# Kernel optimization log

Measured on AMD Instinct MI355X. Metric: run time of the kernel, lower is better.

## Reference

```python
import jax, jax.numpy as jnp
import numpy as np

LN_EPS = 1e-5

def setup_inputs() -> dict:
    key = jax.random.key(0)
    k1, k2, k3 = jax.random.split(key, 3)
    B, Lq, Lk, D = 16, 2048, 2048, 128
    return {
        "query": jax.random.normal(k1, (B, Lq, D), dtype=jnp.float32),
        "key": jax.random.normal(k2, (B, Lk, D), dtype=jnp.float32),
        "value": jax.random.normal(k3, (B, Lk, D), dtype=jnp.float32),
        "attn_mask": jnp.zeros((Lq, Lk), dtype=jnp.float32),
        "gamma": jnp.ones((D,), dtype=jnp.float32),
        "beta": jnp.zeros((D,), dtype=jnp.float32),
    }

def reference(query, key, value, attn_mask, gamma, beta):
    # NOTE: original code does NOT scale by 1/sqrt(d) despite the class name.
    scores = jnp.einsum("bqd,bkd->bqk", query, key)          # [B,Lq,Lk]
    scores = scores + attn_mask[None, :, :]
    probs = jax.nn.softmax(scores, axis=-1)
    out = jnp.einsum("bqk,bkd->bqd", probs, value)            # [B,Lq,D]
    # dropout is identity (eval / rate 0)
    mu = jnp.mean(out, axis=-1, keepdims=True)
    var = jnp.var(out, axis=-1, keepdims=True)
    normed = (out - mu) * jax.lax.rsqrt(var + LN_EPS)
    return normed * gamma + beta
```

## Files before the change

kernel.cpp:

```cpp
#include <hip/hip_runtime.h>
#include <hip/hip_bf16.h>
#include <math.h>

#define LQ_  2048
#define LK_  2048
#define D_   128
#define B_   16
#define LN_EPS 1e-5f
#define TK_  32
#define NTILE (LK_ / TK_)

#define KH_TILE_US 4096
#define VT_TILE_U  2048
#define KH_BYTES   ((size_t)B_ * NTILE * KH_TILE_US * 2)
#define VT_OFF     (2 * KH_BYTES)

typedef __attribute__((ext_vector_type(8))) short short8;
typedef __attribute__((ext_vector_type(4))) float f32x4;

union FragU { uint4 u4; short8 s8; unsigned int u[4]; };

__device__ __forceinline__ unsigned int pk_bf16(float a, float b) {
  __hip_bfloat162 h = __float22bfloat162_rn(make_float2(a, b));
  unsigned int u;
  __builtin_memcpy(&u, &h, 4);
  return u;
}
__device__ __forceinline__ float bf_lo(unsigned int u){ unsigned int v = u << 16; float f; __builtin_memcpy(&f, &v, 4); return f; }
__device__ __forceinline__ float bf_hi(unsigned int u){ unsigned int v = u & 0xffff0000u; float f; __builtin_memcpy(&f, &v, 4); return f; }
__device__ __forceinline__ unsigned short bf16_bits(float x) {
  return (unsigned short)(pk_bf16(x, 0.f) & 0xffffu);
}

__device__ __forceinline__ int idxK(int row, int d) {
  return row * 128 + ((((d >> 3) ^ row) & 15) << 3) + (d & 7);
}
__device__ __forceinline__ int idxVt(int d, int kp) {
  return d * 16 + ((((kp >> 2) + (d >> 1)) & 3) << 2) + (kp & 3);
}
__device__ __forceinline__ int idxPs(int row, int col) {
  return row * 32 + ((((col >> 3) ^ (row >> 2)) & 3) << 3) + (col & 7);
}

__device__ __forceinline__ void barrier_lds() {
  asm volatile("s_waitcnt lgkmcnt(0)\n\ts_barrier" ::: "memory");
}
__device__ __forceinline__ void barrier_stage() {
  asm volatile("s_waitcnt vmcnt(8) lgkmcnt(0)\n\ts_barrier" ::: "memory");
}

__device__ __forceinline__ void gld_lds16(const void* g, void* l) {
  __builtin_amdgcn_global_load_lds((const __attribute__((address_space(1))) void*)g,
                                   (__attribute__((address_space(3))) void*)l, 16, 0, 0);
}

__global__ __launch_bounds__(256) void conv_kv(
    const float* __restrict__ kg, const float* __restrict__ vg,
    unsigned short* __restrict__ khg, unsigned short* __restrict__ klg,
    unsigned int* __restrict__ vtg)
{
  __shared__ float Vlt[128 * 33];
  const int tid = threadIdx.x;
  const int blk = blockIdx.x;
  const int b = blk >> 6;
  const int t = blk & 63;

  const float* ks = kg + ((size_t)b * LK_ + t * 32) * D_;
  const float* vs = vg + ((size_t)b * LK_ + t * 32) * D_;
  unsigned short* kh = khg + (size_t)blk * KH_TILE_US;
  unsigned short* kl = klg + (size_t)blk * KH_TILE_US;
  unsigned int*   vt = vtg + (size_t)blk * VT_TILE_U;

#pragma unroll
  for (int it = 0; it < 2; it++) {
    const int item = tid + it * 256;
    const int row = item >> 4;
    const int c8  = item & 15;
    const float* p = ks + row * D_ + c8 * 8;
    float4 x = *(const float4*)(p);
    float4 y = *(const float4*)(p + 4);
    FragU H, L;
    H.u[0] = pk_bf16(x.x, x.y); H.u[1] = pk_bf16(x.z, x.w);
    H.u[2] = pk_bf16(y.x, y.y); H.u[3] = pk_bf16(y.z, y.w);
    L.u[0] = pk_bf16(x.x - bf_lo(H.u[0]), x.y - bf_hi(H.u[0]));
    L.u[1] = pk_bf16(x.z - bf_lo(H.u[1]), x.w - bf_hi(H.u[1]));
    L.u[2] = pk_bf16(y.x - bf_lo(H.u[2]), y.y - bf_hi(H.u[2]));
    L.u[3] = pk_bf16(y.z - bf_lo(H.u[3]), y.w - bf_hi(H.u[3]));
    const int ik = idxK(row, c8 * 8);
    *(uint4*)&kh[ik] = H.u4;
    *(uint4*)&kl[ik] = L.u4;
  }

#pragma unroll
  for (int i = 0; i < 4; i++) {
    const int item = tid + i * 256;
    const int r = item >> 5, c4 = item & 31;
    float4 x = *(const float4*)&vs[r * D_ + c4 * 4];
    Vlt[(c4 * 4 + 0) * 33 + r] = x.x;
    Vlt[(c4 * 4 + 1) * 33 + r] = x.y;
    Vlt[(c4 * 4 + 2) * 33 + r] = x.z;
    Vlt[(c4 * 4 + 3) * 33 + r] = x.w;
  }
  __syncthreads();

#pragma unroll
  for (int i = 0; i < 8; i++) {
    const int o = tid + i * 256;
    const int d = o >> 4, s = o & 15;
    const int gq = s >> 2, c = s & 3;
    const int kp = (((gq - (d >> 1)) & 3) << 2) | c;
    vt[o] = pk_bf16(Vlt[d * 33 + 2 * kp], Vlt[d * 33 + 2 * kp + 1]);
  }
}

__device__ __forceinline__ void stage_tile(int w, int lane,
    const unsigned short* khT, const unsigned short* klT, const unsigned int* vtT,
    int tile, unsigned short* khs, unsigned short* kls, unsigned int* vts)
{
  const char* gkh = (const char*)(khT + (size_t)tile * KH_TILE_US);
  const char* gkl = (const char*)(klT + (size_t)tile * KH_TILE_US);
  const char* gvt = (const char*)(vtT + (size_t)tile * VT_TILE_U);
#pragma unroll
  for (int c = 0; c < 2; c++) {
    const int off = (w + 4 * c) << 10;
    gld_lds16(gkh + off + lane * 16, (char*)khs + off);
    gld_lds16(gkl + off + lane * 16, (char*)kls + off);
    gld_lds16(gvt + off + lane * 16, (char*)vts + off);
  }
}

__global__ __launch_bounds__(256, 2) void attn_ln_mfma(
    const float* __restrict__ qg, const float* __restrict__ maskg,
    const float* __restrict__ gammag, const float* __restrict__ betag,
    const unsigned short* __restrict__ khg, const unsigned short* __restrict__ klg,
    const unsigned int* __restrict__ vtg,
    float* __restrict__ outg)
{
  __shared__ unsigned short KhS[2][32 * 128];
  __shared__ unsigned short KlS[2][32 * 128];
  __shared__ unsigned int   VtW[2][128 * 16];
  __shared__ unsigned short PsS[64 * 32];

  float* lExch = (float*)&PsS[0];
  float* sExch = ((float*)&PsS[0]) + 128;

  const int tid  = threadIdx.x;
  const int w    = tid >> 6;
  const int lane = tid & 63;
  const int quad = lane >> 4;
  const int lr   = lane & 15;
  const int rowgrp = w & 1;
  const int khalf  = w >> 1;

  const int id   = blockIdx.x;
  const int xcd  = id & 7;
  const int slot = id >> 3;
  const int b    = xcd * 2 + (slot >> 5);
  const int q0   = (slot & 31) * 64;

  const unsigned short* khT = khg + (size_t)b * NTILE * KH_TILE_US;
  const unsigned short* klT = klg + (size_t)b * NTILE * KH_TILE_US;
  const unsigned int*   vtT = vtg + (size_t)b * NTILE * VT_TILE_U;

  const float* mbase = maskg + (size_t)(q0 + rowgrp * 32 + quad * 4) * LK_ + khalf * 16 + lr;

  stage_tile(w, lane, khT, klT, vtT, 0, &KhS[0][0], &KlS[0][0], &VtW[0][0]);
  float mA[2][4], mB[2][4];
#pragma unroll
  for (int rt = 0; rt < 2; rt++)
#pragma unroll
    for (int reg = 0; reg < 4; reg++)
      mA[rt][reg] = mbase[(size_t)(rt * 16 + reg) * LK_];

  short8 qh[2][4], ql[2][4];
#pragma unroll
  for (int rt = 0; rt < 2; rt++) {
    const float* qrow = qg + ((size_t)b * LQ_ + q0 + rowgrp * 32 + rt * 16 + lr) * D_ + quad * 8;
#pragma unroll
    for (int c = 0; c < 4; c++) {
      float4 x = *(const float4*)(qrow + c * 32);
      float4 y = *(const float4*)(qrow + c * 32 + 4);
      FragU H, L;
      H.u[0] = pk_bf16(x.x, x.y); H.u[1] = pk_bf16(x.z, x.w);
      H.u[2] = pk_bf16(y.x, y.y); H.u[3] = pk_bf16(y.z, y.w);
      L.u[0] = pk_bf16(x.x - bf_lo(H.u[0]), x.y - bf_hi(H.u[0]));
      L.u[1] = pk_bf16(x.z - bf_lo(H.u[1]), x.w - bf_hi(H.u[1]));
      L.u[2] = pk_bf16(y.x - bf_lo(H.u[2]), y.y - bf_hi(H.u[2]));
      L.u[3] = pk_bf16(y.z - bf_lo(H.u[3]), y.w - bf_hi(H.u[3]));
      qh[rt][c] = H.s8; ql[rt][c] = L.s8;
    }
  }

  float l_part[2][4];
  f32x4 o[2][4];
  const f32x4 zf = {0.f, 0.f, 0.f, 0.f};
#pragma unroll
  for (int rt = 0; rt < 2; rt++) {
#pragma unroll
    for (int r = 0; r < 4; r++) l_part[rt][r] = 0.f;
#pragma unroll
    for (int n = 0; n < 4; n++) o[rt][n] = zf;
  }

  auto body = [&](int kt, int cur, float (&mu)[2][4], float (&mp)[2][4])
      __attribute__((always_inline)) -> void {
    const unsigned short* khc = &KhS[cur][0];
    const unsigned short* klc = &KlS[cur][0];
    const unsigned int*   vtc = &VtW[cur][0];

    barrier_stage();

    if (kt + 1 < NTILE) {
      stage_tile(w, lane, khT, klT, vtT, kt + 1,
                 &KhS[cur ^ 1][0], &KlS[cur ^ 1][0], &VtW[cur ^ 1][0]);
#pragma unroll
      for (int rt = 0; rt < 2; rt++)
#pragma unroll
        for (int reg = 0; reg < 4; reg++)
          mp[rt][reg] = mbase[(size_t)(rt * 16 + reg) * LK_ + (kt + 1) * TK_];
    }

    f32x4 sacc[2];
    sacc[0] = zf; sacc[1] = zf;
#pragma unroll
    for (int c = 0; c < 4; c++) {
      const int kb = c * 32 + quad * 8;
      const int krow = khalf * 16 + lr;
      FragU kh, kl;
      kh.u4 = *(const uint4*)&khc[idxK(krow, kb)];
      kl.u4 = *(const uint4*)&klc[idxK(krow, kb)];
#pragma unroll
      for (int rt = 0; rt < 2; rt++) {
        sacc[rt] = __builtin_amdgcn_mfma_f32_16x16x32_bf16(qh[rt][c], kh.s8, sacc[rt], 0, 0, 0);
        sacc[rt] = __builtin_amdgcn_mfma_f32_16x16x32_bf16(ql[rt][c], kh.s8, sacc[rt], 0, 0, 0);
        sacc[rt] = __builtin_amdgcn_mfma_f32_16x16x32_bf16(qh[rt][c], kl.s8, sacc[rt], 0, 0, 0);
      }
    }

    FragU Bv[4];
#pragma unroll
    for (int nb = 0; nb < 4; nb++)
      Bv[nb].u4 = *(const uint4*)&vtc[idxVt(khalf * 64 + nb * 16 + lr, quad * 4)];

#pragma unroll
    for (int rt = 0; rt < 2; rt++)
#pragma unroll
      for (int reg = 0; reg < 4; reg++) {
        float p = __expf(sacc[rt][reg] + mu[rt][reg]);
        l_part[rt][reg] += p;
        PsS[idxPs(rowgrp * 32 + rt * 16 + quad * 4 + reg, khalf * 16 + lr)] = bf16_bits(p);
      }

    barrier_lds();

#pragma unroll
    for (int rt = 0; rt < 2; rt++) {
      FragU A;
      A.u4 = *(const uint4*)&PsS[idxPs(rowgrp * 32 + rt * 16 + lr, quad * 8)];
#pragma unroll
      for (int nb = 0; nb < 4; nb++)
        o[rt][nb] = __builtin_amdgcn_mfma_f32_16x16x32_bf16(A.s8, Bv[nb].s8, o[rt][nb], 0, 0, 0);
    }
  };

  for (int kt = 0; kt < NTILE; kt += 2) {
    body(kt,     0, mA, mB);
    body(kt + 1, 1, mB, mA);
  }

  barrier_lds();

  float lred[2][4];
#pragma unroll
  for (int rt = 0; rt < 2; rt++)
#pragma unroll
    for (int reg = 0; reg < 4; reg++) {
      float l = l_part[rt][reg];
#pragma unroll
      for (int m = 1; m <= 8; m <<= 1) l += __shfl_xor(l, m, 64);
      lred[rt][reg] = l;
    }
  if (lr == 0) {
#pragma unroll
    for (int rt = 0; rt < 2; rt++)
#pragma unroll
      for (int reg = 0; reg < 4; reg++)
        lExch[khalf * 64 + rowgrp * 32 + rt * 16 + quad * 4 + reg] = lred[rt][reg];
  }
  barrier_lds();

  float inv_l[2][4];
#pragma unroll
  for (int rt = 0; rt < 2; rt++)
#pragma unroll
    for (int reg = 0; reg < 4; reg++) {
      const int row = rowgrp * 32 + rt * 16 + quad * 4 + reg;
      inv_l[rt][reg] = 1.f / (lred[rt][reg] + lExch[(1 ^ khalf) * 64 + row]);
    }

  float s1p[2][4], s2p[2][4];
#pragma unroll
  for (int rt = 0; rt < 2; rt++)
#pragma unroll
    for (int reg = 0; reg < 4; reg++) {
      float s1 = 0.f, s2 = 0.f;
#pragma unroll
      for (int nb = 0; nb < 4; nb++) {
        float v = o[rt][nb][reg] * inv_l[rt][reg];
        o[rt][nb][reg] = v;
        s1 += v; s2 += v * v;
      }
#pragma unroll
      for (int m = 1; m <= 8; m <<= 1) {
        s1 += __shfl_xor(s1, m, 64);
        s2 += __shfl_xor(s2, m, 64);
      }
      s1p[rt][reg] = s1; s2p[rt][reg] = s2;
    }
  if (lr == 0) {
#pragma unroll
    for (int rt = 0; rt < 2; rt++)
#pragma unroll
      for (int reg = 0; reg < 4; reg++) {
        const int row = rowgrp * 32 + rt * 16 + quad * 4 + reg;
        sExch[(khalf * 64 + row) * 2 + 0] = s1p[rt][reg];
        sExch[(khalf * 64 + row) * 2 + 1] = s2p[rt][reg];
      }
  }
  barrier_lds();

  float gam[4], bet[4];
#pragma unroll
  for (int nb = 0; nb < 4; nb++) {
    gam[nb] = gammag[khalf * 64 + nb * 16 + lr];
    bet[nb] = betag[khalf * 64 + nb * 16 + lr];
  }

#pragma unroll
  for (int rt = 0; rt < 2; rt++)
#pragma unroll
    for (int reg = 0; reg < 4; reg++) {
      const int row = rowgrp * 32 + rt * 16 + quad * 4 + reg;
      const float s1 = s1p[rt][reg] + sExch[((1 ^ khalf) * 64 + row) * 2 + 0];
      const float s2 = s2p[rt][reg] + sExch[((1 ^ khalf) * 64 + row) * 2 + 1];
      const float mean = s1 * (1.f / 128.f);
      const float var  = s2 * (1.f / 128.f) - mean * mean;
      const float rstd = rsqrtf(var + LN_EPS);

      float* op = outg + ((size_t)b * LQ_ + q0 + row) * D_ + khalf * 64 + lr;
#pragma unroll
      for (int nb = 0; nb < 4; nb++)
        op[nb * 16] = (o[rt][nb][reg] - mean) * rstd * gam[nb] + bet[nb];
    }
}

extern "C" void kernel_launch(void* const* d_in, const int* in_sizes, int n_in,
                              void* d_out, int out_size, void* d_ws, size_t ws_size,
                              hipStream_t stream) {
  const float* q     = (const float*)d_in[0];
  const float* k     = (const float*)d_in[1];
  const float* v     = (const float*)d_in[2];
  const float* mask  = (const float*)d_in[3];
  const float* gamma = (const float*)d_in[4];
  const float* beta  = (const float*)d_in[5];
  float* out = (float*)d_out;

  unsigned short* khg = (unsigned short*)d_ws;
  unsigned short* klg = (unsigned short*)((char*)d_ws + KH_BYTES);
  unsigned int*   vtg = (unsigned int*)((char*)d_ws + VT_OFF);

  conv_kv<<<dim3(B_ * NTILE), dim3(256), 0, stream>>>(k, v, khg, klg, vtg);
  attn_ln_mfma<<<dim3(512), dim3(256), 0, stream>>>(q, mask, gamma, beta,
                                                    khg, klg, vtg, out);
}
```

Baseline: 196.5 us.

## Give each wave 16 full query rows to drop cross-wave P exchange barriers

Work is split differently across waves: each of the four waves now owns 16 query rows across all 32 keys of the tile and all 128 output columns, instead of a 2x2 split of rows and key halves. The P tile each wave writes to LDS is read back only by that same wave, so the per-tile block barrier becomes a local lgkmcnt wait. The final softmax-sum and LayerNorm reductions no longer need LDS exchanges or barriers. The QK product also uses three independent accumulators (hi*hi, lo*hi, hi*lo) to shorten MFMA dependency chains. In exchange each wave issues twice the K LDS reads and keeps eight output accumulators live, which raises register pressure at two blocks per CU.

```diff
diff --git a/kernel.cpp b/kernel.cpp
--- a/kernel.cpp
+++ b/kernel.cpp
@@ -42,11 +42,11 @@
   return row * 32 + ((((col >> 3) ^ (row >> 2)) & 3) << 3) + (col & 7);
 }
 
-__device__ __forceinline__ void barrier_lds() {
-  asm volatile("s_waitcnt lgkmcnt(0)\n\ts_barrier" ::: "memory");
-}
 __device__ __forceinline__ void barrier_stage() {
   asm volatile("s_waitcnt vmcnt(8) lgkmcnt(0)\n\ts_barrier" ::: "memory");
+}
+__device__ __forceinline__ void fence_lds_local() {
+  asm volatile("s_waitcnt lgkmcnt(0)" ::: "memory");
 }
 
 __device__ __forceinline__ void gld_lds16(const void* g, void* l) {
@@ -141,16 +141,11 @@
   __shared__ unsigned int   VtW[2][128 * 16];
   __shared__ unsigned short PsS[64 * 32];
 
-  float* lExch = (float*)&PsS[0];
-  float* sExch = ((float*)&PsS[0]) + 128;
-
   const int tid  = threadIdx.x;
   const int w    = tid >> 6;
   const int lane = tid & 63;
   const int quad = lane >> 4;
   const int lr   = lane & 15;
-  const int rowgrp = w & 1;
-  const int khalf  = w >> 1;
 
   const int id   = blockIdx.x;
   const int xcd  = id & 7;
@@ -162,20 +157,19 @@
   const unsigned short* klT = klg + (size_t)b * NTILE * KH_TILE_US;
   const unsigned int*   vtT = vtg + (size_t)b * NTILE * VT_TILE_U;
 
-  const float* mbase = maskg + (size_t)(q0 + rowgrp * 32 + quad * 4) * LK_ + khalf * 16 + lr;
+  const float* mbase = maskg + (size_t)(q0 + w * 16 + quad * 4) * LK_ + lr;
 
   stage_tile(w, lane, khT, klT, vtT, 0, &KhS[0][0], &KlS[0][0], &VtW[0][0]);
   float mA[2][4], mB[2][4];
 #pragma unroll
-  for (int rt = 0; rt < 2; rt++)
+  for (int ct = 0; ct < 2; ct++)
 #pragma unroll
     for (int reg = 0; reg < 4; reg++)
-      mA[rt][reg] = mbase[(size_t)(rt * 16 + reg) * LK_];
-
-  short8 qh[2][4], ql[2][4];
-#pragma unroll
-  for (int rt = 0; rt < 2; rt++) {
-    const float* qrow = qg + ((size_t)b * LQ_ + q0 + rowgrp * 32 + rt * 16 + lr) * D_ + quad * 8;
+      mA[ct][reg] = mbase[(size_t)reg * LK_ + ct * 16];
+
+  short8 qh[4], ql[4];
+  {
+    const float* qrow = qg + ((size_t)b * LQ_ + q0 + w * 16 + lr) * D_ + quad * 8;
 #pragma unroll
     for (int c = 0; c < 4; c++) {
       float4 x = *(const float4*)(qrow + c * 32);
@@ -187,20 +181,15 @@
       L.u[1] = pk_bf16(x.z - bf_lo(H.u[1]), x.w - bf_hi(H.u[1]));
       L.u[2] = pk_bf16(y.x - bf_lo(H.u[2]), y.y - bf_hi(H.u[2]));
       L.u[3] = pk_bf16(y.z - bf_lo(H.u[3]), y.w - bf_hi(H.u[3]));
-      qh[rt][c] = H.s8; ql[rt][c] = L.s8;
-    }
-  }
-
-  float l_part[2][4];
-  f32x4 o[2][4];
+      qh[c] = H.s8; ql[c] = L.s8;
+    }
+  }
+
+  float l_part[4] = {0.f, 0.f, 0.f, 0.f};
+  f32x4 o[8];
   const f32x4 zf = {0.f, 0.f, 0.f, 0.f};
 #pragma unroll
-  for (int rt = 0; rt < 2; rt++) {
-#pragma unroll
-    for (int r = 0; r < 4; r++) l_part[rt][r] = 0.f;
-#pragma unroll
-    for (int n = 0; n < 4; n++) o[rt][n] = zf;
-  }
+  for (int n = 0; n < 8; n++) o[n] = zf;
 
   auto body = [&](int kt, int cur, float (&mu)[2][4], float (&mp)[2][4])
       __attribute__((always_inline)) -> void {
@@ -214,53 +203,50 @@
       stage_tile(w, lane, khT, klT, vtT, kt + 1,
                  &KhS[cur ^ 1][0], &KlS[cur ^ 1][0], &VtW[cur ^ 1][0]);
 #pragma unroll
-      for (int rt = 0; rt < 2; rt++)
+      for (int ct = 0; ct < 2; ct++)
 #pragma unroll
         for (int reg = 0; reg < 4; reg++)
-          mp[rt][reg] = mbase[(size_t)(rt * 16 + reg) * LK_ + (kt + 1) * TK_];
-    }
-
-    f32x4 sacc[2];
-    sacc[0] = zf; sacc[1] = zf;
+          mp[ct][reg] = mbase[(size_t)reg * LK_ + (kt + 1) * TK_ + ct * 16];
+    }
+
+    f32x4 sH[2], sL[2], sM[2];
+    sH[0] = zf; sH[1] = zf; sL[0] = zf; sL[1] = zf; sM[0] = zf; sM[1] = zf;
 #pragma unroll
     for (int c = 0; c < 4; c++) {
-      const int kb = c * 32 + quad * 8;
-      const int krow = khalf * 16 + lr;
-      FragU kh, kl;
-      kh.u4 = *(const uint4*)&khc[idxK(krow, kb)];
-      kl.u4 = *(const uint4*)&klc[idxK(krow, kb)];
-#pragma unroll
-      for (int rt = 0; rt < 2; rt++) {
-        sacc[rt] = __builtin_amdgcn_mfma_f32_16x16x32_bf16(qh[rt][c], kh.s8, sacc[rt], 0, 0, 0);
-        sacc[rt] = __builtin_amdgcn_mfma_f32_16x16x32_bf16(ql[rt][c], kh.s8, sacc[rt], 0, 0, 0);
-        sacc[rt] = __builtin_amdgcn_mfma_f32_16x16x32_bf16(qh[rt][c], kl.s8, sacc[rt], 0, 0, 0);
+#pragma unroll
+      for (int ct = 0; ct < 2; ct++) {
+        const int ik = idxK(ct * 16 + lr, c * 32 + quad * 8);
+        FragU kh, kl;
+        kh.u4 = *(const uint4*)&khc[ik];
+        kl.u4 = *(const uint4*)&klc[ik];
+        sH[ct] = __builtin_amdgcn_mfma_f32_16x16x32_bf16(qh[c], kh.s8, sH[ct], 0, 0, 0);
+        sL[ct] = __builtin_amdgcn_mfma_f32_16x16x32_bf16(ql[c], kh.s8, sL[ct], 0, 0, 0);
+        sM[ct] = __builtin_amdgcn_mfma_f32_16x16x32_bf16(qh[c], kl.s8, sM[ct], 0, 0, 0);
       }
     }
 
-    FragU Bv[4];
-#pragma unroll
-    for (int nb = 0; nb < 4; nb++)
-      Bv[nb].u4 = *(const uint4*)&vtc[idxVt(khalf * 64 + nb * 16 + lr, quad * 4)];
-
-#pragma unroll
-    for (int rt = 0; rt < 2; rt++)
+    FragU Bv[8];
+#pragma unroll
+    for (int nb = 0; nb < 8; nb++)
+      Bv[nb].u4 = *(const uint4*)&vtc[idxVt(nb * 16 + lr, quad * 4)];
+
+#pragma unroll
+    for (int ct = 0; ct < 2; ct++)
 #pragma unroll
       for (int reg = 0; reg < 4; reg++) {
-        float p = __expf(sacc[rt][reg] + mu[rt][reg]);
-        l_part[rt][reg] += p;
-        PsS[idxPs(rowgrp * 32 + rt * 16 + quad * 4 + reg, khalf * 16 + lr)] = bf16_bits(p);
+        float s = sH[ct][reg] + sL[ct][reg] + sM[ct][reg];
+        float p = __expf(s + mu[ct][reg]);
+        l_part[reg] += p;
+        PsS[idxPs(w * 16 + quad * 4 + reg, ct * 16 + lr)] = bf16_bits(p);
       }
 
-    barrier_lds();
-
-#pragma unroll
-    for (int rt = 0; rt < 2; rt++) {
-      FragU A;
-      A.u4 = *(const uint4*)&PsS[idxPs(rowgrp * 32 + rt * 16 + lr, quad * 8)];
-#pragma unroll
-      for (int nb = 0; nb < 4; nb++)
-        o[rt][nb] = __builtin_amdgcn_mfma_f32_16x16x32_bf16(A.s8, Bv[nb].s8, o[rt][nb], 0, 0, 0);
-    }
+    fence_lds_local();
+
+    FragU A;
+    A.u4 = *(const uint4*)&PsS[idxPs(w * 16 + lr, quad * 8)];
+#pragma unroll
+    for (int nb = 0; nb < 8; nb++)
+      o[nb] = __builtin_amdgcn_mfma_f32_16x16x32_bf16(A.s8, Bv[nb].s8, o[nb], 0, 0, 0);
   };
 
   for (int kt = 0; kt < NTILE; kt += 2) {
@@ -268,90 +254,45 @@
     body(kt + 1, 1, mB, mA);
   }
 
-  barrier_lds();
-
-  float lred[2][4];
-#pragma unroll
-  for (int rt = 0; rt < 2; rt++)
-#pragma unroll
-    for (int reg = 0; reg < 4; reg++) {
-      float l = l_part[rt][reg];
-#pragma unroll
-      for (int m = 1; m <= 8; m <<= 1) l += __shfl_xor(l, m, 64);
-      lred[rt][reg] = l;
-    }
-  if (lr == 0) {
-#pragma unroll
-    for (int rt = 0; rt < 2; rt++)
-#pragma unroll
-      for (int reg = 0; reg < 4; reg++)
-        lExch[khalf * 64 + rowgrp * 32 + rt * 16 + quad * 4 + reg] = lred[rt][reg];
-  }
-  barrier_lds();
-
-  float inv_l[2][4];
-#pragma unroll
-  for (int rt = 0; rt < 2; rt++)
-#pragma unroll
-    for (int reg = 0; reg < 4; reg++) {
-      const int row = rowgrp * 32 + rt * 16 + quad * 4 + reg;
-      inv_l[rt][reg] = 1.f / (lred[rt][reg] + lExch[(1 ^ khalf) * 64 + row]);
-    }
-
-  float s1p[2][4], s2p[2][4];
-#pragma unroll
-  for (int rt = 0; rt < 2; rt++)
-#pragma unroll
-    for (int reg = 0; reg < 4; reg++) {
-      float s1 = 0.f, s2 = 0.f;
-#pragma unroll
-      for (int nb = 0; nb < 4; nb++) {
-        float v = o[rt][nb][reg] * inv_l[rt][reg];
-        o[rt][nb][reg] = v;
-        s1 += v; s2 += v * v;
-      }
-#pragma unroll
-      for (int m = 1; m <= 8; m <<= 1) {
-        s1 += __shfl_xor(s1, m, 64);
-        s2 += __shfl_xor(s2, m, 64);
-      }
-      s1p[rt][reg] = s1; s2p[rt][reg] = s2;
-    }
-  if (lr == 0) {
-#pragma unroll
-    for (int rt = 0; rt < 2; rt++)
-#pragma unroll
-      for (int reg = 0; reg < 4; reg++) {
-        const int row = rowgrp * 32 + rt * 16 + quad * 4 + reg;
-        sExch[(khalf * 64 + row) * 2 + 0] = s1p[rt][reg];
-        sExch[(khalf * 64 + row) * 2 + 1] = s2p[rt][reg];
-      }
-  }
-  barrier_lds();
-
-  float gam[4], bet[4];
-#pragma unroll
-  for (int nb = 0; nb < 4; nb++) {
-    gam[nb] = gammag[khalf * 64 + nb * 16 + lr];
-    bet[nb] = betag[khalf * 64 + nb * 16 + lr];
-  }
-
-#pragma unroll
-  for (int rt = 0; rt < 2; rt++)
-#pragma unroll
-    for (int reg = 0; reg < 4; reg++) {
-      const int row = rowgrp * 32 + rt * 16 + quad * 4 + reg;
-      const float s1 = s1p[rt][reg] + sExch[((1 ^ khalf) * 64 + row) * 2 + 0];
-      const float s2 = s2p[rt][reg] + sExch[((1 ^ khalf) * 64 + row) * 2 + 1];
-      const float mean = s1 * (1.f / 128.f);
-      const float var  = s2 * (1.f / 128.f) - mean * mean;
-      const float rstd = rsqrtf(var + LN_EPS);
-
-      float* op = outg + ((size_t)b * LQ_ + q0 + row) * D_ + khalf * 64 + lr;
-#pragma unroll
-      for (int nb = 0; nb < 4; nb++)
-        op[nb * 16] = (o[rt][nb][reg] - mean) * rstd * gam[nb] + bet[nb];
-    }
+  float inv_l[4];
+#pragma unroll
+  for (int reg = 0; reg < 4; reg++) {
+    float l = l_part[reg];
+#pragma unroll
+    for (int m = 1; m <= 8; m <<= 1) l += __shfl_xor(l, m, 64);
+    inv_l[reg] = 1.f / l;
+  }
+
+  float gam[8], bet[8];
+#pragma unroll
+  for (int nb = 0; nb < 8; nb++) {
+    gam[nb] = gammag[nb * 16 + lr];
+    bet[nb] = betag[nb * 16 + lr];
+  }
+
+#pragma unroll
+  for (int reg = 0; reg < 4; reg++) {
+    float s1 = 0.f, s2 = 0.f;
+#pragma unroll
+    for (int nb = 0; nb < 8; nb++) {
+      float v = o[nb][reg] * inv_l[reg];
+      o[nb][reg] = v;
+      s1 += v; s2 += v * v;
+    }
+#pragma unroll
+    for (int m = 1; m <= 8; m <<= 1) {
+      s1 += __shfl_xor(s1, m, 64);
+      s2 += __shfl_xor(s2, m, 64);
+    }
+    const float mean = s1 * (1.f / 128.f);
+    const float var  = s2 * (1.f / 128.f) - mean * mean;
+    const float rstd = rsqrtf(var + LN_EPS);
+
+    float* op = outg + ((size_t)b * LQ_ + q0 + w * 16 + quad * 4 + reg) * D_ + lr;
+#pragma unroll
+    for (int nb = 0; nb < 8; nb++)
+      op[nb * 16] = (o[nb][reg] - mean) * rstd * gam[nb] + bet[nb];
+  }
 }
 
 extern "C" void kernel_launch(void* const* d_in, const int* in_sizes, int n_in,
```

Result: faster. 192.0 us (-2.3%).
